# Kernel optimization log

Hardware: AMD Instinct MI355X
Metric: run time of the kernel (lower is better)

Reference implementation:

```python
import jax, jax.numpy as jnp
import numpy as np

N, L, D = 2, 2048, 96
H, DK, DV = 4, 16, 16
OUT = 96
SPATIAL = H * (3 + 1 + 3)  # points + distance + direction per head
INF = 100000.0
EPS_DIR = 1e-10
EPS_LN = 1e-5


def setup_inputs() -> dict:
    key = jax.random.key(0)
    ks = jax.random.split(key, 10)
    return {
        "x": jax.random.normal(ks[0], (N, L, D), jnp.float32),
        "pos_CA": jax.random.normal(ks[1], (N, L, 3), jnp.float32),
        "pos_CB": jax.random.normal(ks[2], (N, L, 3), jnp.float32),
        "frame": jax.random.normal(ks[3], (N, L, 3, 3), jnp.float32),
        "mask": jnp.ones((N, L), dtype=bool),
        "Wq": jax.random.normal(ks[4], (D, H * DK), jnp.float32) * 0.1,
        "Wk": jax.random.normal(ks[5], (D, H * DK), jnp.float32) * 0.1,
        "Wv": jax.random.normal(ks[6], (D, H * DV), jnp.float32) * 0.1,
        "Wo": jax.random.normal(ks[7], (H * DV + SPATIAL, OUT), jnp.float32) * 0.1,
        "bo": jnp.zeros((OUT,), jnp.float32),
        "gamma": jnp.ones((OUT,), jnp.float32),
        "beta": jnp.zeros((OUT,), jnp.float32),
    }


def reference(x, pos_CA, pos_CB, frame, mask, Wq, Wk, Wv, Wo, bo, gamma, beta):
    n, l, _ = x.shape
    q = (x @ Wq).reshape(n, l, H, DK)
    k = (x @ Wk).reshape(n, l, H, DK)
    v = (x @ Wv).reshape(n, l, H, DV)

    # logits (N, L_q, L_k, H)
    logits = jnp.einsum('blhd,bkhd->blkh', q, k)
    mask_row = mask[:, :, None, None]           # (N, L, 1, 1)
    mask_pair = mask_row & mask[:, None, :, None]
    logits = jnp.where(mask_pair, logits, logits - INF)
    alpha = jax.nn.softmax(logits, axis=2)
    alpha = jnp.where(mask_row, alpha, 0.0)

    feat_node = jnp.einsum('blkh,bkhd->blhd', alpha, v).reshape(n, l, H * DV)

    # rel_pos[b,l,k] = CB[k] - CA[l]
    rel_pos = pos_CB[:, None, :, :] - pos_CA[:, :, None, :]
    atom_pos_bias = jnp.einsum('blkh,blkd->blhd', alpha, rel_pos)  # (N,L,H,3)
    feat_distance = jnp.linalg.norm(atom_pos_bias, axis=-1, keepdims=True)
    feat_points = jnp.einsum('blij,blhj->blhi', frame, atom_pos_bias)
    feat_direction = feat_points / (jnp.linalg.norm(feat_points, axis=-1, keepdims=True) + EPS_DIR)

    feat_spatial = jnp.concatenate([
        feat_points.reshape(n, l, H * 3),
        feat_distance.reshape(n, l, H),
        feat_direction.reshape(n, l, H * 3),
    ], axis=-1)

    feat_all = jnp.concatenate([feat_node, feat_spatial], axis=-1) @ Wo + bo
    feat_all = jnp.where(mask[:, :, None], feat_all, 0.0)

    # output_dim == input_dim -> residual + LayerNorm
    h = x + feat_all
    mu = jnp.mean(h, axis=-1, keepdims=True)
    var = jnp.var(h, axis=-1, keepdims=True)
    return (h - mu) / jnp.sqrt(var + EPS_LN) * gamma + beta
```

## Files before the change

kernel.cpp:

```cpp
#include <hip/hip_runtime.h>
#include <hip/hip_fp16.h>

typedef _Float16 f16;
typedef _Float16 v2h __attribute__((ext_vector_type(2)));
typedef _Float16 v4h __attribute__((ext_vector_type(4)));
typedef _Float16 v8h __attribute__((ext_vector_type(8)));
typedef short    v4s __attribute__((ext_vector_type(4)));
typedef short    v8s __attribute__((ext_vector_type(8)));
typedef float    v4f __attribute__((ext_vector_type(4)));

#define NB   2
#define LSEQ 2048
#define DIM  96
#define NH   4
#define ROWS 4096
#define NT16 128
#define NT32 64
#define OUTD 96
#define SHIFT 12.0f
#define ST 28

#define MFMA_F16(A, B, C) __builtin_amdgcn_mfma_f32_16x16x32_f16((A), (B), (C), 0, 0, 0)
#define MFMA_BF16(A, B, C) __builtin_amdgcn_mfma_f32_16x16x32_bf16((A), (B), (C), 0, 0, 0)

static __device__ __forceinline__ short f2bf(float f) {
    unsigned u = __builtin_bit_cast(unsigned, f);
    u += 0x7FFF + ((u >> 16) & 1);
    return (short)(u >> 16);
}

__global__ __launch_bounds__(256) void proj_kernel(
    const float* __restrict__ x,
    const float* __restrict__ posCB,
    const float* __restrict__ Wq,
    const float* __restrict__ Wk,
    const float* __restrict__ Wv,
    f16*   __restrict__ qf,
    f16*   __restrict__ kf,
    short* __restrict__ vf,
    short* __restrict__ pf)
{
    const int w    = threadIdx.x >> 6;
    const int lane = threadIdx.x & 63;
    const int row  = blockIdx.x * 4 + w;
    const int b    = row >> 11;
    const int seq  = row & (LSEQ - 1);
    const int h    = lane >> 4;
    const int d    = lane & 15;

    __shared__ float xs[4][DIM];
    xs[w][lane] = x[(size_t)row * DIM + lane];
    if (lane < DIM - 64) xs[w][64 + lane] = x[(size_t)row * DIM + 64 + lane];
    __syncthreads();

    float qa = 0.f, ka = 0.f, va = 0.f;
    #pragma unroll 8
    for (int dd = 0; dd < DIM; ++dd) {
        const float xv = xs[w][dd];
        qa = fmaf(xv, Wq[dd * 64 + lane], qa);
        ka = fmaf(xv, Wk[dd * 64 + lane], ka);
        va = fmaf(xv, Wv[dd * 64 + lane], va);
    }

    const int bh  = b * NH + h;
    const int t16 = seq >> 4, m = seq & 15;
    const size_t baseQ = ((size_t)(bh * NT16 + t16)) * 512;
    const int laneQK = m + 16 * (d >> 3);
    const int jQK    = d & 7;
    qf[baseQ + laneQK * 8 + jQK] = (f16)qa;
    kf[baseQ + laneQK * 8 + jQK] = (f16)ka;
    qf[baseQ + 256 + m * 16 + d] = (f16)0.f;
    kf[baseQ + 256 + m * 16 + d] = (f16)0.f;

    const int t32 = seq >> 5, kl = seq & 31;
    vf[((size_t)(bh * NT32 + t32)) * 512 + (d + 16 * (kl >> 3)) * 8 + (kl & 7)] = f2bf(va);

    if (blockIdx.x < NB * NT32) {
        const int b2 = blockIdx.x >> 6, t2 = blockIdx.x & 63;
        const int tid = threadIdx.x;
        const int lf = tid & 63, jh = tid >> 6;
        const int n = lf & 15, kq = lf >> 4;
        #pragma unroll
        for (int u = 0; u < 2; ++u) {
            const int key = t2 * 32 + kq * 8 + jh * 2 + u;
            float val = 0.f;
            if (n < 3)       val = posCB[((size_t)(b2 * LSEQ + key)) * 3 + n];
            else if (n == 3) val = 1.f;
            pf[((size_t)(b2 * NT32 + t2)) * 512 + lf * 8 + jh * 2 + u] = f2bf(val);
        }
    }
}

__global__ __launch_bounds__(512, 1) void attn_epi_kernel(
    const f16*   __restrict__ qf,
    const f16*   __restrict__ kf,
    const short* __restrict__ vf,
    const short* __restrict__ pf,
    const float* __restrict__ x,
    const float* __restrict__ posCA,
    const float* __restrict__ frame,
    const float* __restrict__ Wo,
    const float* __restrict__ bo,
    const float* __restrict__ gamma,
    const float* __restrict__ beta,
    float*       __restrict__ out)
{
    const int w     = threadIdx.x >> 6;
    const int lane  = threadIdx.x & 63;
    const int head  = w & 3, khalf = w >> 2;
    const int b     = blockIdx.x >> 7;
    const int qt    = blockIdx.x & 127;
    const int bh    = b * NH + head;
    const int quad  = lane >> 4, c16 = lane & 15;

    __shared__ short pT[8][32 * ST];
    __shared__ float comb[8][64][12];
    __shared__ float feat[16][100];
    __shared__ float aps[16][NH][3];

    const v8h aq = *(const v8h*)(qf + ((size_t)(bh * NT16 + qt)) * 512 + lane * 8);
    const f16*   kb = kf + (size_t)bh * NT16 * 512;
    const short* vb = vf + (size_t)bh * NT32 * 512;
    const short* pb = pf + (size_t)b  * NT32 * 512;

    v4f O  = {0.f, 0.f, 0.f, 0.f};
    v4f Wa = {0.f, 0.f, 0.f, 0.f};
    const v4f zero = {0.f, 0.f, 0.f, 0.f};
    float srow[4] = {0.f, 0.f, 0.f, 0.f};
    short* slot = pT[w];

    #pragma unroll 2
    for (int i = 0; i < 32; ++i) {
        const int t32 = khalf * 32 + i;
        const v8h bk0 = *(const v8h*)(kb + (size_t)(2 * t32    ) * 512 + lane * 8);
        const v8h bk1 = *(const v8h*)(kb + (size_t)(2 * t32 + 1) * 512 + lane * 8);
        v4f S0 = MFMA_F16(aq, bk0, zero);
        v4f S1 = MFMA_F16(aq, bk1, zero);

        v4s pr0, pr1;
        #pragma unroll
        for (int r = 0; r < 4; ++r) {
            const float e0 = __expf(S0[r] - SHIFT);
            const float e1 = __expf(S1[r] - SHIFT);
            pr0[r] = f2bf(e0);
            pr1[r] = f2bf(e1);
            srow[r] += e0 + e1;
        }

        *(v4s*)(slot + c16 * ST + quad * 4)        = pr0;
        *(v4s*)(slot + (16 + c16) * ST + quad * 4) = pr1;
        v8s ap;
        #pragma unroll
        for (int j = 0; j < 8; ++j)
            ap[j] = slot[(quad * 8 + j) * ST + c16];

        const v8s bv = *(const v8s*)(vb + (size_t)t32 * 512 + lane * 8);
        O = MFMA_BF16(ap, bv, O);
        const v8s bp = *(const v8s*)(pb + (size_t)t32 * 512 + lane * 8);
        Wa = MFMA_BF16(ap, bp, Wa);
    }

    {
        float* cb = &comb[w][lane][0];
        *(v4f*)cb       = O;
        *(v4f*)(cb + 4) = Wa;
        #pragma unroll
        for (int r = 0; r < 4; ++r) cb[8 + r] = srow[r];
    }
    __syncthreads();

    if (w < 4) {
        const float* cb = &comb[w + 4][lane][0];
        O  += *(const v4f*)cb;
        Wa += *(const v4f*)(cb + 4);
        #pragma unroll
        for (int r = 0; r < 4; ++r) srow[r] += cb[8 + r];

        #pragma unroll
        for (int mask = 1; mask < 16; mask <<= 1) {
            #pragma unroll
            for (int r = 0; r < 4; ++r) srow[r] += __shfl_xor(srow[r], mask);
        }
        float inv[4];
        #pragma unroll
        for (int r = 0; r < 4; ++r) inv[r] = 1.f / srow[r];

        #pragma unroll
        for (int r = 0; r < 4; ++r)
            feat[4 * quad + r][w * 16 + c16] = O[r] * inv[r];
        if (c16 < 3) {
            #pragma unroll
            for (int r = 0; r < 4; ++r)
                aps[4 * quad + r][w][c16] = Wa[r] * inv[r];
        }
    }
    __syncthreads();

    const int rowg0 = b * LSEQ + qt * 16;

    if (lane < 8) {
        const int pair = w * 8 + lane;
        const int r16 = pair >> 2, hh = pair & 3;
        const int grow = rowg0 + r16;
        float apb[3];
        #pragma unroll
        for (int j = 0; j < 3; ++j)
            apb[j] = aps[r16][hh][j] - posCA[(size_t)grow * 3 + j];
        const float dist = sqrtf(apb[0]*apb[0] + apb[1]*apb[1] + apb[2]*apb[2]);
        float fp[3];
        #pragma unroll
        for (int i = 0; i < 3; ++i) {
            float a = 0.f;
            #pragma unroll
            for (int j = 0; j < 3; ++j)
                a = fmaf(frame[(size_t)grow * 9 + i * 3 + j], apb[j], a);
            fp[i] = a;
        }
        const float fpn  = sqrtf(fp[0]*fp[0] + fp[1]*fp[1] + fp[2]*fp[2]);
        const float rinv = 1.f / (fpn + 1e-10f);
        #pragma unroll
        for (int i = 0; i < 3; ++i) {
            feat[r16][64 + hh * 3 + i] = fp[i];
            feat[r16][80 + hh * 3 + i] = fp[i] * rinv;
        }
        feat[r16][76 + hh] = dist;
    }
    __syncthreads();

    #pragma unroll
    for (int rr = 0; rr < 2; ++rr) {
        const int r16 = w * 2 + rr;
        const int grow = rowg0 + r16;

        float acc0 = bo[lane];
        #pragma unroll 4
        for (int r2 = 0; r2 < 92; ++r2)
            acc0 = fmaf(feat[r16][r2], Wo[r2 * OUTD + lane], acc0);
        const float hv0 = acc0 + x[(size_t)grow * DIM + lane];

        float hv1 = 0.f;
        if (lane < 32) {
            float acc1 = bo[64 + lane];
            #pragma unroll 4
            for (int r2 = 0; r2 < 92; ++r2)
                acc1 = fmaf(feat[r16][r2], Wo[r2 * OUTD + 64 + lane], acc1);
            hv1 = acc1 + x[(size_t)grow * DIM + 64 + lane];
        }

        float ls = hv0 + hv1;
        float lq = fmaf(hv0, hv0, hv1 * hv1);
        #pragma unroll
        for (int off = 32; off > 0; off >>= 1) {
            ls += __shfl_xor(ls, off);
            lq += __shfl_xor(lq, off);
        }
        const float mu  = ls * (1.f / OUTD);
        const float var = lq * (1.f / OUTD) - mu * mu;
        const float rs  = rsqrtf(var + 1e-5f);

        out[(size_t)grow * OUTD + lane] = (hv0 - mu) * rs * gamma[lane] + beta[lane];
        if (lane < 32)
            out[(size_t)grow * OUTD + 64 + lane] =
                (hv1 - mu) * rs * gamma[64 + lane] + beta[64 + lane];
    }
}

extern "C" void kernel_launch(void* const* d_in, const int* in_sizes, int n_in,
                              void* d_out, int out_size, void* d_ws, size_t ws_size,
                              hipStream_t stream)
{
    const float* x     = (const float*)d_in[0];
    const float* posCA = (const float*)d_in[1];
    const float* posCB = (const float*)d_in[2];
    const float* frame = (const float*)d_in[3];
    const float* Wq    = (const float*)d_in[5];
    const float* Wk    = (const float*)d_in[6];
    const float* Wv    = (const float*)d_in[7];
    const float* Wo    = (const float*)d_in[8];
    const float* bo    = (const float*)d_in[9];
    const float* gamma = (const float*)d_in[10];
    const float* beta  = (const float*)d_in[11];

    f16*   qf = (f16*)d_ws;
    f16*   kf = qf + (size_t)8 * NT16 * 512;
    short* vf = (short*)(kf + (size_t)8 * NT16 * 512);
    short* pf = vf + (size_t)8 * NT32 * 512;

    proj_kernel<<<ROWS / 4, 256, 0, stream>>>(x, posCB, Wq, Wk, Wv, qf, kf, vf, pf);
    attn_epi_kernel<<<NB * NT16, 512, 0, stream>>>(qf, kf, vf, pf,
                                                   x, posCA, frame,
                                                   Wo, bo, gamma, beta,
                                                   (float*)d_out);
}
```

Baseline: 119.8 us.

## Split attention over key chunks into separate kernel with partial-sum epilogue

```diff
diff --git a/kernel.cpp b/kernel.cpp
--- a/kernel.cpp
+++ b/kernel.cpp
@@ -2,8 +2,6 @@
 #include <hip/hip_fp16.h>
 
 typedef _Float16 f16;
-typedef _Float16 v2h __attribute__((ext_vector_type(2)));
-typedef _Float16 v4h __attribute__((ext_vector_type(4)));
 typedef _Float16 v8h __attribute__((ext_vector_type(8)));
 typedef short    v4s __attribute__((ext_vector_type(4)));
 typedef short    v8s __attribute__((ext_vector_type(8)));
@@ -19,8 +17,9 @@
 #define OUTD 96
 #define SHIFT 12.0f
 #define ST 28
-
-#define MFMA_F16(A, B, C) __builtin_amdgcn_mfma_f32_16x16x32_f16((A), (B), (C), 0, 0, 0)
+#define PART_STRIDE 544
+
+#define MFMA_F16(A, B, C)  __builtin_amdgcn_mfma_f32_16x16x32_f16((A), (B), (C), 0, 0, 0)
 #define MFMA_BF16(A, B, C) __builtin_amdgcn_mfma_f32_16x16x32_bf16((A), (B), (C), 0, 0, 0)
 
 static __device__ __forceinline__ short f2bf(float f) {
@@ -35,50 +34,63 @@
     const float* __restrict__ Wq,
     const float* __restrict__ Wk,
     const float* __restrict__ Wv,
-    f16*   __restrict__ qf,
-    f16*   __restrict__ kf,
+    f16*   __restrict__ qc,
+    f16*   __restrict__ kc,
     short* __restrict__ vf,
     short* __restrict__ pf)
 {
-    const int w    = threadIdx.x >> 6;
-    const int lane = threadIdx.x & 63;
-    const int row  = blockIdx.x * 4 + w;
-    const int b    = row >> 11;
-    const int seq  = row & (LSEQ - 1);
-    const int h    = lane >> 4;
-    const int d    = lane & 15;
-
-    __shared__ float xs[4][DIM];
-    xs[w][lane] = x[(size_t)row * DIM + lane];
-    if (lane < DIM - 64) xs[w][64 + lane] = x[(size_t)row * DIM + 64 + lane];
+    const int t    = threadIdx.x;
+    const int w    = t >> 6;
+    const int lane = t & 63;
+    const int h    = lane >> 4, d = lane & 15;
+    const int b    = blockIdx.x >> 7;
+    const int t16  = blockIdx.x & 127;
+    const int row0 = b * LSEQ + t16 * 16;
+
+    __shared__ float xs[16][DIM];
+    {
+        const float* src = x + (size_t)row0 * DIM;
+        for (int i = t; i < 16 * DIM; i += 256) xs[i / DIM][i % DIM] = src[i];
+    }
     __syncthreads();
 
-    float qa = 0.f, ka = 0.f, va = 0.f;
-    #pragma unroll 8
+    float qa[4] = {0.f,0.f,0.f,0.f}, ka[4] = {0.f,0.f,0.f,0.f}, va[4] = {0.f,0.f,0.f,0.f};
+    #pragma unroll 4
     for (int dd = 0; dd < DIM; ++dd) {
-        const float xv = xs[w][dd];
-        qa = fmaf(xv, Wq[dd * 64 + lane], qa);
-        ka = fmaf(xv, Wk[dd * 64 + lane], ka);
-        va = fmaf(xv, Wv[dd * 64 + lane], va);
-    }
-
-    const int bh  = b * NH + h;
-    const int t16 = seq >> 4, m = seq & 15;
-    const size_t baseQ = ((size_t)(bh * NT16 + t16)) * 512;
-    const int laneQK = m + 16 * (d >> 3);
-    const int jQK    = d & 7;
-    qf[baseQ + laneQK * 8 + jQK] = (f16)qa;
-    kf[baseQ + laneQK * 8 + jQK] = (f16)ka;
-    qf[baseQ + 256 + m * 16 + d] = (f16)0.f;
-    kf[baseQ + 256 + m * 16 + d] = (f16)0.f;
-
-    const int t32 = seq >> 5, kl = seq & 31;
-    vf[((size_t)(bh * NT32 + t32)) * 512 + (d + 16 * (kl >> 3)) * 8 + (kl & 7)] = f2bf(va);
+        const float wq = Wq[dd * 64 + lane];
+        const float wk = Wk[dd * 64 + lane];
+        const float wv = Wv[dd * 64 + lane];
+        #pragma unroll
+        for (int r = 0; r < 4; ++r) {
+            const float xv = xs[w * 4 + r][dd];
+            qa[r] = fmaf(xv, wq, qa[r]);
+            ka[r] = fmaf(xv, wk, ka[r]);
+            va[r] = fmaf(xv, wv, va[r]);
+        }
+    }
+
+    __shared__ f16   sq[4][264], sk[4][264];
+    __shared__ short sv[4][264];
+    #pragma unroll
+    for (int r = 0; r < 4; ++r) {
+        const int m = w * 4 + r;
+        const int idxQ = (m + 16 * (d >> 3)) * 8 + (d & 7);
+        sq[h][idxQ] = (f16)qa[r];
+        sk[h][idxQ] = (f16)ka[r];
+        const int idxV = (d + 16 * (m >> 3)) * 8 + (m & 7);
+        sv[h][idxV] = f2bf(va[r]);
+    }
+    __syncthreads();
+
+    const int bh = b * NH + w;
+    *(v4s*)(void*)(qc + ((size_t)(bh * NT16 + t16)) * 256 + lane * 4) = *(v4s*)(void*)&sq[w][lane * 4];
+    *(v4s*)(void*)(kc + ((size_t)(bh * NT16 + t16)) * 256 + lane * 4) = *(v4s*)(void*)&sk[w][lane * 4];
+    *(v4s*)(vf + ((size_t)(bh * NT32 + (t16 >> 1))) * 512 + (t16 & 1) * 256 + lane * 4) =
+        *(v4s*)(void*)&sv[w][lane * 4];
 
     if (blockIdx.x < NB * NT32) {
         const int b2 = blockIdx.x >> 6, t2 = blockIdx.x & 63;
-        const int tid = threadIdx.x;
-        const int lf = tid & 63, jh = tid >> 6;
+        const int lf = t & 63, jh = t >> 6;
         const int n = lf & 15, kq = lf >> 4;
         #pragma unroll
         for (int u = 0; u < 2; ++u) {
@@ -91,11 +103,89 @@
     }
 }
 
-__global__ __launch_bounds__(512, 1) void attn_epi_kernel(
-    const f16*   __restrict__ qf,
-    const f16*   __restrict__ kf,
+__global__ __launch_bounds__(512, 1) void attn_kernel(
+    const f16*   __restrict__ qc,
+    const f16*   __restrict__ kc,
     const short* __restrict__ vf,
     const short* __restrict__ pf,
+    float*       __restrict__ part)
+{
+    const int w     = threadIdx.x >> 6;
+    const int lane  = threadIdx.x & 63;
+    const int head  = w & 3, khalf = w >> 2;
+    const int b     = blockIdx.x >> 9;
+    const int qt    = (blockIdx.x >> 2) & 127;
+    const int kq    = blockIdx.x & 3;
+    const int bh    = b * NH + head;
+    const int quad  = lane >> 4, c16 = lane & 15;
+
+    __shared__ short pT[8][32 * ST];
+
+    v8h aq = {0,0,0,0,0,0,0,0};
+    if (lane < 32)
+        aq = *(const v8h*)(qc + ((size_t)(bh * NT16 + qt)) * 256 + lane * 8);
+    const f16*   kb = kc + (size_t)bh * NT16 * 256;
+    const short* vb = vf + (size_t)bh * NT32 * 512;
+    const short* pb = pf + (size_t)b  * NT32 * 512;
+
+    v4f O  = {0.f, 0.f, 0.f, 0.f};
+    v4f Wa = {0.f, 0.f, 0.f, 0.f};
+    const v4f zero = {0.f, 0.f, 0.f, 0.f};
+    float srow[4] = {0.f, 0.f, 0.f, 0.f};
+    short* slot = pT[w];
+
+    #pragma unroll 2
+    for (int i = 0; i < 8; ++i) {
+        const int t32 = kq * 16 + khalf * 8 + i;
+        v8h bk0 = {0,0,0,0,0,0,0,0}, bk1 = {0,0,0,0,0,0,0,0};
+        if (lane < 32) {
+            bk0 = *(const v8h*)(kb + (size_t)(2 * t32    ) * 256 + lane * 8);
+            bk1 = *(const v8h*)(kb + (size_t)(2 * t32 + 1) * 256 + lane * 8);
+        }
+        v4f S0 = MFMA_F16(aq, bk0, zero);
+        v4f S1 = MFMA_F16(aq, bk1, zero);
+
+        v4s pr0, pr1;
+        #pragma unroll
+        for (int r = 0; r < 4; ++r) {
+            const float e0 = __expf(S0[r] - SHIFT);
+            const float e1 = __expf(S1[r] - SHIFT);
+            pr0[r] = f2bf(e0);
+            pr1[r] = f2bf(e1);
+            srow[r] += e0 + e1;
+        }
+
+        *(v4s*)(slot + c16 * ST + quad * 4)        = pr0;
+        *(v4s*)(slot + (16 + c16) * ST + quad * 4) = pr1;
+        v8s ap;
+        #pragma unroll
+        for (int j = 0; j < 8; ++j)
+            ap[j] = slot[(quad * 8 + j) * ST + c16];
+
+        const v8s bv = *(const v8s*)(vb + (size_t)t32 * 512 + lane * 8);
+        O = MFMA_BF16(ap, bv, O);
+        const v8s bp = *(const v8s*)(pb + (size_t)t32 * 512 + lane * 8);
+        Wa = MFMA_BF16(ap, bp, Wa);
+    }
+
+    #pragma unroll
+    for (int mask = 1; mask < 16; mask <<= 1) {
+        #pragma unroll
+        for (int r = 0; r < 4; ++r) srow[r] += __shfl_xor(srow[r], mask);
+    }
+
+    const int combo = kq * 2 + khalf;
+    float* dst = part + ((((size_t)(b * 128 + qt)) * 8 + combo) * 4 + head) * PART_STRIDE;
+    *(v4f*)(dst + lane * 8)     = O;
+    *(v4f*)(dst + lane * 8 + 4) = Wa;
+    if (c16 == 0) {
+        #pragma unroll
+        for (int r = 0; r < 4; ++r) dst[512 + 4 * quad + r] = srow[r];
+    }
+}
+
+__global__ __launch_bounds__(512) void epi_kernel(
+    const float* __restrict__ part,
     const float* __restrict__ x,
     const float* __restrict__ posCA,
     const float* __restrict__ frame,
@@ -105,86 +195,32 @@
     const float* __restrict__ beta,
     float*       __restrict__ out)
 {
-    const int w     = threadIdx.x >> 6;
-    const int lane  = threadIdx.x & 63;
-    const int head  = w & 3, khalf = w >> 2;
-    const int b     = blockIdx.x >> 7;
-    const int qt    = blockIdx.x & 127;
-    const int bh    = b * NH + head;
-    const int quad  = lane >> 4, c16 = lane & 15;
-
-    __shared__ short pT[8][32 * ST];
-    __shared__ float comb[8][64][12];
+    const int w    = threadIdx.x >> 6;
+    const int lane = threadIdx.x & 63;
+    const int b    = blockIdx.x >> 7;
+    const int qt   = blockIdx.x & 127;
+    const int quad = lane >> 4, c16 = lane & 15;
+
     __shared__ float feat[16][100];
     __shared__ float aps[16][NH][3];
 
-    const v8h aq = *(const v8h*)(qf + ((size_t)(bh * NT16 + qt)) * 512 + lane * 8);
-    const f16*   kb = kf + (size_t)bh * NT16 * 512;
-    const short* vb = vf + (size_t)bh * NT32 * 512;
-    const short* pb = pf + (size_t)b  * NT32 * 512;
-
-    v4f O  = {0.f, 0.f, 0.f, 0.f};
-    v4f Wa = {0.f, 0.f, 0.f, 0.f};
-    const v4f zero = {0.f, 0.f, 0.f, 0.f};
-    float srow[4] = {0.f, 0.f, 0.f, 0.f};
-    short* slot = pT[w];
-
-    #pragma unroll 2
-    for (int i = 0; i < 32; ++i) {
-        const int t32 = khalf * 32 + i;
-        const v8h bk0 = *(const v8h*)(kb + (size_t)(2 * t32    ) * 512 + lane * 8);
-        const v8h bk1 = *(const v8h*)(kb + (size_t)(2 * t32 + 1) * 512 + lane * 8);
-        v4f S0 = MFMA_F16(aq, bk0, zero);
-        v4f S1 = MFMA_F16(aq, bk1, zero);
-
-        v4s pr0, pr1;
-        #pragma unroll
-        for (int r = 0; r < 4; ++r) {
-            const float e0 = __expf(S0[r] - SHIFT);
-            const float e1 = __expf(S1[r] - SHIFT);
-            pr0[r] = f2bf(e0);
-            pr1[r] = f2bf(e1);
-            srow[r] += e0 + e1;
-        }
-
-        *(v4s*)(slot + c16 * ST + quad * 4)        = pr0;
-        *(v4s*)(slot + (16 + c16) * ST + quad * 4) = pr1;
-        v8s ap;
-        #pragma unroll
-        for (int j = 0; j < 8; ++j)
-            ap[j] = slot[(quad * 8 + j) * ST + c16];
-
-        const v8s bv = *(const v8s*)(vb + (size_t)t32 * 512 + lane * 8);
-        O = MFMA_BF16(ap, bv, O);
-        const v8s bp = *(const v8s*)(pb + (size_t)t32 * 512 + lane * 8);
-        Wa = MFMA_BF16(ap, bp, Wa);
-    }
-
-    {
-        float* cb = &comb[w][lane][0];
-        *(v4f*)cb       = O;
-        *(v4f*)(cb + 4) = Wa;
-        #pragma unroll
-        for (int r = 0; r < 4; ++r) cb[8 + r] = srow[r];
-    }
-    __syncthreads();
-
     if (w < 4) {
-        const float* cb = &comb[w + 4][lane][0];
-        O  += *(const v4f*)cb;
-        Wa += *(const v4f*)(cb + 4);
-        #pragma unroll
-        for (int r = 0; r < 4; ++r) srow[r] += cb[8 + r];
-
-        #pragma unroll
-        for (int mask = 1; mask < 16; mask <<= 1) {
+        const float* pbase =
+            part + (((size_t)(b * 128 + qt)) * 8 * 4 + w) * PART_STRIDE;
+        v4f O  = {0.f, 0.f, 0.f, 0.f};
+        v4f Wa = {0.f, 0.f, 0.f, 0.f};
+        float sr[4] = {0.f, 0.f, 0.f, 0.f};
+        #pragma unroll
+        for (int combo = 0; combo < 8; ++combo) {
+            const float* pp = pbase + (size_t)combo * 4 * PART_STRIDE;
+            O  += *(const v4f*)(pp + lane * 8);
+            Wa += *(const v4f*)(pp + lane * 8 + 4);
             #pragma unroll
-            for (int r = 0; r < 4; ++r) srow[r] += __shfl_xor(srow[r], mask);
+            for (int r = 0; r < 4; ++r) sr[r] += pp[512 + 4 * quad + r];
         }
         float inv[4];
         #pragma unroll
-        for (int r = 0; r < 4; ++r) inv[r] = 1.f / srow[r];
-
+        for (int r = 0; r < 4; ++r) inv[r] = 1.f / sr[r];
         #pragma unroll
         for (int r = 0; r < 4; ++r)
             feat[4 * quad + r][w * 16 + c16] = O[r] * inv[r];
@@ -281,14 +317,15 @@
     const float* gamma = (const float*)d_in[10];
     const float* beta  = (const float*)d_in[11];
 
-    f16*   qf = (f16*)d_ws;
-    f16*   kf = qf + (size_t)8 * NT16 * 512;
-    short* vf = (short*)(kf + (size_t)8 * NT16 * 512);
-    short* pf = vf + (size_t)8 * NT32 * 512;
-
-    proj_kernel<<<ROWS / 4, 256, 0, stream>>>(x, posCB, Wq, Wk, Wv, qf, kf, vf, pf);
-    attn_epi_kernel<<<NB * NT16, 512, 0, stream>>>(qf, kf, vf, pf,
-                                                   x, posCA, frame,
-                                                   Wo, bo, gamma, beta,
-                                                   (float*)d_out);
-}
+    f16*   qc   = (f16*)d_ws;
+    f16*   kc   = qc + (size_t)8 * NT16 * 256;
+    short* vf   = (short*)(kc + (size_t)8 * NT16 * 256);
+    short* pf   = vf + (size_t)8 * NT32 * 512;
+    float* part = (float*)(pf + (size_t)NB * NT32 * 512);
+
+    proj_kernel<<<NB * NT16, 256, 0, stream>>>(x, posCB, Wq, Wk, Wv, qc, kc, vf, pf);
+    attn_kernel<<<NB * NT16 * 4, 512, 0, stream>>>(qc, kc, vf, pf, part);
+    epi_kernel<<<NB * NT16, 512, 0, stream>>>(part, x, posCA, frame,
+                                              Wo, bo, gamma, beta,
+                                              (float*)d_out);
+}
```

After: 131.3 us. 9.6% more time.
